# Kernel tuning notes

Measured on AMD Instinct MI355X. Metric: run time of the kernel, lower is better.

Reference implementation:

```python
import jax, jax.numpy as jnp
import numpy as np

# ---- static skeleton configuration ----
TOPOLOGY = [[0,1],[1,2],[2,3],[3,4],[0,5],[5,6],[6,7],[7,8],[0,9],[9,10],[10,11],[11,12],
            [12,13],[13,14],[12,15],[15,16],[16,17],[17,18],[18,19],[12,20],[20,21],[21,22],[22,23],[23,24]]
NEIGHBOUR_LIST = [[0,1,2,4,5,8,9,24],[0,1,2,3,4,8],[0,1,2,3],[1,2,3],[0,1,4,5,6,8,9,24],[0,4,5,6,7,8],
                  [4,5,6,7],[5,6,7],[0,1,4,5,8,9,10,24],[0,4,8,9,10,11],[8,9,10,11,12,14,19],
                  [9,10,11,12,13,14,15,19,20],[10,11,12,13,14,15,19,20],[11,12,13,14,19],
                  [10,11,12,13,14,15,16,19,20],[11,12,14,15,16,17,19],[14,15,16,17,18],[15,16,17,18],
                  [16,17,18],[10,11,12,13,14,15,19,20,21],[11,12,14,19,20,21,22],[19,20,21,22,23],
                  [20,21,22,23],[21,22,23],[0,4,8,24]]
JOINT_NUM, IN_C, OUT_C, K, STRIDE, PAD = 25, 200, 400, 3, 2, 1
GN_GROUPS, GN_EPS = 10, 1e-5

def build_mask(nbr_list, in_c, out_c, joint_num, k):
    cin, cout = in_c // joint_num, out_c // joint_num
    m = np.zeros((out_c, in_c, k), np.float32)
    for i, nbr in enumerate(nbr_list):
        cols = [j * cin + c for j in nbr for c in range(cin)]
        m[i * cout:(i + 1) * cout, cols, :] = 1.0
    return jnp.asarray(m)

def build_pool(edges, cpe):
    edge_num = len(edges) + 1
    deg = {}
    for a, b in edges:
        deg[a] = deg.get(a, 0) + 1; deg[b] = deg.get(b, 0) + 1
    seq_list = []
    def find_seq(j, seq):
        if deg[j] > 2 and j != 0:
            seq_list.append(seq); seq = []
        if deg[j] == 1:
            seq_list.append(seq); return
        for idx, (a, b) in enumerate(edges):
            if a == j:
                find_seq(b, seq + [idx])
    find_seq(0, [])
    pooling_list = []
    for seq in seq_list:
        if len(seq) % 2 == 1:
            pooling_list.append([seq[0]]); seq = seq[1:]
        for i in range(0, len(seq), 2):
            pooling_list.append([seq[i], seq[i + 1]])
    pooling_list.append([edge_num - 1])
    W = np.zeros((len(pooling_list) * cpe, edge_num * cpe), np.float32)
    for i, pair in enumerate(pooling_list):
        for j in pair:
            W[i * cpe:(i + 1) * cpe, j * cpe:(j + 1) * cpe] += np.eye(cpe, dtype=np.float32) / len(pair)
    return jnp.asarray(W)

MASK0 = build_mask(NEIGHBOUR_LIST, IN_C, IN_C, JOINT_NUM, K)    # extra conv in->in
MASK1 = build_mask(NEIGHBOUR_LIST, IN_C, OUT_C, JOINT_NUM, K)   # main conv in->out
MASK_SC = build_mask(NEIGHBOUR_LIST, IN_C, OUT_C, JOINT_NUM, 1) # shortcut k=1
POOL_W = build_pool(TOPOLOGY, OUT_C // JOINT_NUM)               # [224, 400]

def conv1d(x, w, b, stride, pad):
    if pad > 0:
        x = jnp.pad(x, ((0, 0), (0, 0), (pad, pad)), mode='reflect')
    y = jax.lax.conv_general_dilated(x, w, (stride,), 'VALID',
                                     dimension_numbers=('NCH', 'OIH', 'NCH'))
    return y + b[None, :, None]

def group_norm(x, gamma, beta):
    B, C, T = x.shape
    xg = x.reshape(B, GN_GROUPS, C // GN_GROUPS, T)
    mu = xg.mean((2, 3), keepdims=True)
    var = xg.var((2, 3), keepdims=True)
    xn = ((xg - mu) * jax.lax.rsqrt(var + GN_EPS)).reshape(B, C, T)
    return xn * gamma[None, :, None] + beta[None, :, None]

def prelu(x, a):
    return jnp.where(x >= 0, x, a[0] * x)

def setup_inputs() -> dict:
    key = jax.random.key(0)
    ks = jax.random.split(key, 8)
    return {
        'x': jax.random.normal(ks[0], (16, IN_C, 8192), jnp.float32),
        'w0': jax.random.normal(ks[1], (IN_C, IN_C, K), jnp.float32) * 0.05,
        'b0': jax.random.normal(ks[2], (IN_C,), jnp.float32) * 0.05,
        'a0': jnp.full((1,), 0.25, jnp.float32),
        'w1': jax.random.normal(ks[3], (OUT_C, IN_C, K), jnp.float32) * 0.05,
        'b1': jax.random.normal(ks[4], (OUT_C,), jnp.float32) * 0.05,
        'gn_gamma': jnp.ones((OUT_C,), jnp.float32),
        'gn_beta': jnp.zeros((OUT_C,), jnp.float32),
        'ws': jax.random.normal(ks[5], (OUT_C, IN_C, 1), jnp.float32) * 0.05,
        'bs': jax.random.normal(ks[6], (OUT_C,), jnp.float32) * 0.05,
        'a1': jnp.full((1,), 0.25, jnp.float32),
    }

def reference(x, w0, b0, a0, w1, b1, gn_gamma, gn_beta, ws, bs, a1):
    # residual branch: extra SkeletonConv + PReLU, SkeletonConv (stride 2), GroupNorm
    h = conv1d(x, w0 * MASK0, b0, 1, PAD)
    h = prelu(h, a0)
    h = conv1d(h, w1 * MASK1, b1, STRIDE, PAD)
    h = group_norm(h, gn_gamma, gn_beta)
    # shortcut: masked 1x1 conv, stride 2
    s = conv1d(x, ws * MASK_SC, bs, STRIDE, 0)
    out = h + s                                   # [B, 400, 4096]
    out = jnp.einsum('nc,bct->bnt', POOL_W, out)  # SkeletonPool mean -> [B, 224, 4096]
    return prelu(out, a1)
```

## Files before the change

### kernel.cpp

```cpp
#include <hip/hip_runtime.h>

#define BATCH 16
#define CIN   200
#define T1    8192
#define COUTC 400
#define TT2   4096
#define NJ    25
#define NGROUP 10
#define CPG   40
#define NPOOL 14
#define CROWB 528

typedef __attribute__((ext_vector_type(8))) short bf16x8;
typedef __attribute__((ext_vector_type(4))) float f32x4;

__constant__ int NBR_OFF[NJ + 1] = {0,8,14,18,21,29,35,39,42,50,56,63,72,80,85,94,101,106,110,113,122,129,134,138,141,145};
__constant__ int NBR[145] = {
 0,1,2,4,5,8,9,24,
 0,1,2,3,4,8,
 0,1,2,3,
 1,2,3,
 0,1,4,5,6,8,9,24,
 0,4,5,6,7,8,
 4,5,6,7,
 5,6,7,
 0,1,4,5,8,9,10,24,
 0,4,8,9,10,11,
 8,9,10,11,12,14,19,
 9,10,11,12,13,14,15,19,20,
 10,11,12,13,14,15,19,20,
 11,12,13,14,19,
 10,11,12,13,14,15,16,19,20,
 11,12,14,15,16,17,19,
 14,15,16,17,18,
 15,16,17,18,
 16,17,18,
 10,11,12,13,14,15,19,20,21,
 11,12,14,19,20,21,22,
 19,20,21,22,23,
 20,21,22,23,
 21,22,23,
 0,4,8,24};
__constant__ int PAIR_A[NPOOL] = {0,2,4,6,8,10,12,14,15,17,19,20,22,24};
__constant__ int PAIR_B[NPOOL] = {1,3,5,7,9,11,13,-1,16,18,-1,21,23,-1};
__constant__ int JSPLIT[5] = {0,6,12,18,25};
__constant__ int PUOFF[15] = {0,9,13,22,26,35,45,53,62,70,74,83,91,95,99};
__constant__ int PU[99] = {
 0,1,2,3,4,5,8,9,24,
 0,1,2,3,
 0,1,4,5,6,7,8,9,24,
 4,5,6,7,
 0,1,4,5,8,9,10,11,24,
 8,9,10,11,12,13,14,15,19,20,
 10,11,12,13,14,15,19,20,
 10,11,12,13,14,15,16,19,20,
 11,12,14,15,16,17,18,19,
 15,16,17,18,
 10,11,12,13,14,15,19,20,21,
 11,12,14,19,20,21,22,23,
 20,21,22,23,
 0,4,8,24};
__constant__ int PNMF[NPOOL] = {7,3,7,3,7,8,6,7,6,3,7,6,3,3};
__constant__ int FB0[NPOOL]  = {0,7,10,17,20,27,35,41,48,54,57,64,70,73};
__constant__ int FRAG_P[76] = {
 0,0,0,0,0,0,0, 1,1,1, 2,2,2,2,2,2,2, 3,3,3, 4,4,4,4,4,4,4, 5,5,5,5,5,5,5,5,
 6,6,6,6,6,6, 7,7,7,7,7,7,7, 8,8,8,8,8,8, 9,9,9, 10,10,10,10,10,10,10,
 11,11,11,11,11,11, 12,12,12, 13,13,13};
__constant__ int NSF[NJ] = {2,2,1,1,2,2,1,1,2,2,2,3,2,2,3,2,2,1,1,3,2,2,1,1,1};
__constant__ int FBS[NJ] = {0,2,4,5,6,8,10,11,12,14,16,18,21,23,25,28,30,32,33,34,37,39,41,42,43};
__constant__ int FRAG_SJ[44] = {
 0,0, 1,1, 2, 3, 4,4, 5,5, 6, 7, 8,8, 9,9, 10,10, 11,11,11, 12,12, 13,13,
 14,14,14, 15,15, 16,16, 17, 18, 19,19,19, 20,20, 21,21, 22, 23, 24};
#define NF1   (NJ * 7)
#define DSC_SC   304
#define DSC_C1   480
#define DSC_TOT  (DSC_C1 + NF1 * 4)

__device__ __forceinline__ unsigned bfround(float f) {
    unsigned u = __builtin_bit_cast(unsigned, f);
    return (u + 0x7FFFu + ((u >> 16) & 1u)) >> 16;
}
__device__ __forceinline__ unsigned packbf(float lo, float hi) {
    return bfround(lo) | (bfround(hi) << 16);
}
__device__ __forceinline__ float bflo(unsigned u) { return __builtin_bit_cast(float, u << 16); }
__device__ __forceinline__ float bfhi(unsigned u) { return __builtin_bit_cast(float, u & 0xFFFF0000u); }

__global__ void wprep1(const float* __restrict__ w1, unsigned short* __restrict__ wA)
{
    const int f  = blockIdx.x;
    const int jo = f / 7;
    const int mf = f - jo * 7;
    const int off = NBR_OFF[jo];
    const int deg = NBR_OFF[jo + 1] - off;
    for (int e = threadIdx.x; e < 512; e += 256) {
        int lane = e >> 3, j = e & 7;
        int m = lane & 15, kb = lane >> 4;
        int c8 = mf * 4 + kb;
        float v = 0.f;
        if (c8 < 3 * deg) {
            int tap = (c8 >= 2 * deg) ? 2 : ((c8 >= deg) ? 1 : 0);
            int nbr_i = c8 - tap * deg;
            int ci = NBR[off + nbr_i] * 8 + j;
            v = w1[(size_t)(jo * 16 + m) * 600 + ci * 3 + tap];
        }
        wA[(size_t)f * 512 + e] = (unsigned short)bfround(v);
    }
}

__global__ void wprep0(const float* __restrict__ w0, unsigned short* __restrict__ wA)
{
    const int f  = blockIdx.x;
    const int p  = FRAG_P[f];
    const int mf = f - FB0[p];
    const int puo = PUOFF[p];
    const int u   = PUOFF[p + 1] - puo;
    for (int e = threadIdx.x; e < 512; e += 256) {
        int lane = e >> 3, j = e & 7;
        int m = lane & 15, kb = lane >> 4;
        int c8 = mf * 4 + kb;
        int jm = (m < 8) ? PAIR_A[p] : PAIR_B[p];
        float v = 0.f;
        if (c8 < 3 * u && jm >= 0) {
            int tap = (c8 >= 2 * u) ? 2 : ((c8 >= u) ? 1 : 0);
            int ni  = c8 - tap * u;
            int nbr = PU[puo + ni];
            int offj = NBR_OFF[jm], degj = NBR_OFF[jm + 1] - offj;
            bool mem = false;
            for (int s = 0; s < degj; ++s) mem = mem || (NBR[offj + s] == nbr);
            if (mem) {
                int ci = nbr * 8 + j;
                v = w0[(size_t)(jm * 8 + (m & 7)) * 600 + ci * 3 + tap];
            }
        }
        wA[(size_t)f * 512 + e] = (unsigned short)bfround(v);
    }
}

__global__ void wprepS(const float* __restrict__ wsc, unsigned short* __restrict__ wA)
{
    const int f  = blockIdx.x;
    const int jo = FRAG_SJ[f];
    const int mf = f - FBS[jo];
    const int off = NBR_OFF[jo];
    const int deg = NBR_OFF[jo + 1] - off;
    for (int e = threadIdx.x; e < 512; e += 256) {
        int lane = e >> 3, j = e & 7;
        int m = lane & 15, kb = lane >> 4;
        int c8 = mf * 4 + kb;
        float v = 0.f;
        if (c8 < deg) {
            int ci = NBR[off + c8] * 8 + j;
            v = wsc[(size_t)(jo * 16 + m) * 200 + ci];
        }
        wA[(size_t)f * 512 + e] = (unsigned short)bfround(v);
    }
}

__global__ void dprep(int* __restrict__ dsc)
{
    for (int e = threadIdx.x; e < DSC_TOT; e += 256) {
        if (e < DSC_SC) {
            int f = e >> 2, q = e & 3;
            int p = FRAG_P[f], mf = f - FB0[p];
            int puo = PUOFF[p], u = PUOFF[p + 1] - puo;
            int c8 = mf * 4 + q;
            int tp = 0, ni = 0;
            if (c8 < 3 * u) {
                tp = (c8 >= 2 * u) ? 2 : ((c8 >= u) ? 1 : 0);
                ni = c8 - tp * u;
            }
            dsc[e] = (tp << 12) | (PU[puo + ni] * 16);
        } else if (e < DSC_C1) {
            int e2 = e - DSC_SC;
            int f = e2 >> 2, q = e2 & 3;
            int jo = FRAG_SJ[f], mf = f - FBS[jo];
            int off = NBR_OFF[jo], deg = NBR_OFF[jo + 1] - off;
            int c8 = mf * 4 + q;
            int ni = (c8 < deg) ? c8 : deg - 1;
            dsc[e] = NBR[off + ni] * 16;
        } else {
            int e2 = e - DSC_C1;
            int f = e2 >> 2, q = e2 & 3;
            int jo = f / 7, mf = f - jo * 7;
            int off = NBR_OFF[jo], deg = NBR_OFF[jo + 1] - off;
            int c8 = mf * 4 + q;
            int tp = 0, ni = 0;
            if (c8 < 3 * deg) {
                tp = (c8 >= 2 * deg) ? 2 : ((c8 >= deg) ? 1 : 0);
                ni = c8 - tp * deg;
            }
            int rowd = (tp == 1) ? 33 : (tp >> 1);
            dsc[e] = rowd * CROWB + NBR[off + ni] * 16;
        }
    }
}

__global__ __launch_bounds__(256) void conv0s_mfma(
    const float* __restrict__ x, const unsigned short* __restrict__ wA0,
    const unsigned short* __restrict__ wAs, const int* __restrict__ dsc,
    const float* __restrict__ b0, const float* __restrict__ a0,
    const float* __restrict__ bsc,
    unsigned short* __restrict__ h0T, unsigned short* __restrict__ sbu)
{
    __shared__ __align__(16) unsigned short xs[66 * 264];
    __shared__ int dl[DSC_C1];
    __shared__ float b0l[CIN], bscl[COUTC];
    const int b   = blockIdx.y;
    const int t0  = blockIdx.x * 64;
    const int tid = threadIdx.x;

    for (int i = tid; i < DSC_C1; i += 256) dl[i] = dsc[i];
    for (int i = tid; i < CIN; i += 256) b0l[i] = b0[i];
    for (int i = tid; i < COUTC; i += 256) bscl[i] = bsc[i];

    const float* xb = x + (size_t)b * CIN * T1;
    for (int e = tid; e < (CIN / 4) * 16; e += 256) {
        int c4 = e >> 4, k = e & 15;
        const float* xc = xb + (size_t)(4 * c4) * T1 + t0 + 4 * k;
        float4 v0 = *(const float4*)(xc);
        float4 v1 = *(const float4*)(xc + T1);
        float4 v2 = *(const float4*)(xc + 2 * T1);
        float4 v3 = *(const float4*)(xc + 3 * T1);
        char* base = (char*)xs + 8 * c4 + (4 * k + 1) * CROWB;
        *(uint2*)(base)             = make_uint2(packbf(v0.x, v1.x), packbf(v2.x, v3.x));
        *(uint2*)(base + CROWB)     = make_uint2(packbf(v0.y, v1.y), packbf(v2.y, v3.y));
        *(uint2*)(base + 2 * CROWB) = make_uint2(packbf(v0.z, v1.z), packbf(v2.z, v3.z));
        *(uint2*)(base + 3 * CROWB) = make_uint2(packbf(v0.w, v1.w), packbf(v2.w, v3.w));
    }
    for (int e = tid; e < 2 * CIN; e += 256) {
        int c = e >> 1, h = e & 1;
        int t = h ? (t0 + 64) : (t0 - 1);
        t = (t < 0) ? 1 : ((t >= T1) ? (2 * T1 - 2 - t) : t);
        float v = xb[(size_t)c * T1 + t];
        *(unsigned short*)((char*)xs + (h ? 65 : 0) * CROWB + 2 * c) = (unsigned short)bfround(v);
    }
    __syncthreads();

    const int w = tid >> 6, lane = tid & 63;
    const int q = lane >> 4, n = lane & 15;
    const float alpha = a0[0];
    const int ws2 = w & 1, wh = w >> 1;
    const int pbase = wh * 7;
    const int rA = ws2 * 32 + n;
    char* xsb = (char*)xs + rA * CROWB;

    unsigned h0k[7][2][2];
    for (int pi = 0; pi < 7; ++pi) {
        const int p = pbase + pi;
        const int fb = FB0[p], nmf = PNMF[p];
        const unsigned short* wAb = wA0 + (size_t)fb * 512;
        f32x4 acc0 = {0.f, 0.f, 0.f, 0.f};
        f32x4 acc1 = {0.f, 0.f, 0.f, 0.f};
        int i1 = (nmf > 1) ? 1 : 0;
        bf16x8 af0 = *(const bf16x8*)(wAb + (size_t)lane * 8);
        int d = dl[fb * 4 + q];
        bf16x8 b0v = *(const bf16x8*)(xsb + (d >> 12) * CROWB + (d & 0xFFF));
        bf16x8 b1v = *(const bf16x8*)(xsb + (d >> 12) * CROWB + (d & 0xFFF) + 16 * CROWB);
        bf16x8 af1 = *(const bf16x8*)(wAb + ((size_t)i1 * 64 + lane) * 8);
        d = dl[(fb + i1) * 4 + q];
        bf16x8 b0n = *(const bf16x8*)(xsb + (d >> 12) * CROWB + (d & 0xFFF));
        bf16x8 b1n = *(const bf16x8*)(xsb + (d >> 12) * CROWB + (d & 0xFFF) + 16 * CROWB);
        for (int mf = 0; mf < nmf; ++mf) {
            int m2 = (mf + 2 < nmf) ? mf + 2 : nmf - 1;
            bf16x8 a2 = *(const bf16x8*)(wAb + ((size_t)m2 * 64 + lane) * 8);
            d = dl[(fb + m2) * 4 + q];
            bf16x8 b02 = *(const bf16x8*)(xsb + (d >> 12) * CROWB + (d & 0xFFF));
            bf16x8 b12 = *(const bf16x8*)(xsb + (d >> 12) * CROWB + (d & 0xFFF) + 16 * CROWB);
            acc0 = __builtin_amdgcn_mfma_f32_16x16x32_bf16(af0, b0v, acc0, 0, 0, 0);
            acc1 = __builtin_amdgcn_mfma_f32_16x16x32_bf16(af0, b1v, acc1, 0, 0, 0);
            af0 = af1; af1 = a2;
            b0v = b0n; b0n = b02;
            b1v = b1n; b1n = b12;
        }
        int jm = (q < 2) ? PAIR_A[p] : PAIR_B[p];
        if (jm >= 0) {
            int ocb = (q & 1) * 4;
            float bb0 = b0l[jm * 8 + ocb + 0], bb1 = b0l[jm * 8 + ocb + 1];
            float bb2 = b0l[jm * 8 + ocb + 2], bb3 = b0l[jm * 8 + ocb + 3];
            float v0 = acc0[0] + bb0; v0 = (v0 >= 0.f) ? v0 : alpha * v0;
            float v1 = acc0[1] + bb1; v1 = (v1 >= 0.f) ? v1 : alpha * v1;
            float v2 = acc0[2] + bb2; v2 = (v2 >= 0.f) ? v2 : alpha * v2;
            float v3 = acc0[3] + bb3; v3 = (v3 >= 0.f) ? v3 : alpha * v3;
            h0k[pi][0][0] = packbf(v0, v1); h0k[pi][0][1] = packbf(v2, v3);
            v0 = acc1[0] + bb0; v0 = (v0 >= 0.f) ? v0 : alpha * v0;
            v1 = acc1[1] + bb1; v1 = (v1 >= 0.f) ? v1 : alpha * v1;
            v2 = acc1[2] + bb2; v2 = (v2 >= 0.f) ? v2 : alpha * v2;
            v3 = acc1[3] + bb3; v3 = (v3 >= 0.f) ? v3 : alpha * v3;
            h0k[pi][1][0] = packbf(v0, v1); h0k[pi][1][1] = packbf(v2, v3);
        }
    }

    for (int jo = w; jo < NJ; jo += 4) {
        const int fb = FBS[jo], nsf = NSF[jo];
        const unsigned short* wAb = wAs + (size_t)fb * 512;
        const int dbase = DSC_SC + fb * 4 + q;
        char* rb0 = (char*)xs + (2 * n + 1) * CROWB;
        f32x4 acc0 = {0.f, 0.f, 0.f, 0.f};
        f32x4 acc1 = {0.f, 0.f, 0.f, 0.f};
        int i1 = (nsf > 1) ? 1 : 0;
        bf16x8 af0 = *(const bf16x8*)(wAb + (size_t)lane * 8);
        int d = dl[dbase];
        bf16x8 b0v = *(const bf16x8*)(rb0 + d);
        bf16x8 b1v = *(const bf16x8*)(rb0 + d + 32 * CROWB);
        bf16x8 af1 = *(const bf16x8*)(wAb + ((size_t)i1 * 64 + lane) * 8);
        d = dl[dbase + i1 * 4];
        bf16x8 b0n = *(const bf16x8*)(rb0 + d);
        bf16x8 b1n = *(const bf16x8*)(rb0 + d + 32 * CROWB);
        for (int mf = 0; mf < nsf; ++mf) {
            int m2 = (mf + 2 < nsf) ? mf + 2 : nsf - 1;
            bf16x8 a2 = *(const bf16x8*)(wAb + ((size_t)m2 * 64 + lane) * 8);
            d = dl[dbase + m2 * 4];
            bf16x8 b02 = *(const bf16x8*)(rb0 + d);
            bf16x8 b12 = *(const bf16x8*)(rb0 + d + 32 * CROWB);
            acc0 = __builtin_amdgcn_mfma_f32_16x16x32_bf16(af0, b0v, acc0, 0, 0, 0);
            acc1 = __builtin_amdgcn_mfma_f32_16x16x32_bf16(af0, b1v, acc1, 0, 0, 0);
            af0 = af1; af1 = a2;
            b0v = b0n; b0n = b02;
            b1v = b1n; b1n = b12;
        }
        unsigned short* sp = sbu + ((size_t)b * COUTC + jo * 16 + q * 4) * TT2 + (t0 >> 1) + n;
#pragma unroll
        for (int r = 0; r < 4; ++r) {
            float bsv = bscl[jo * 16 + q * 4 + r];
            sp[(size_t)r * TT2]      = (unsigned short)bfround(acc0[r] + bsv);
            sp[(size_t)r * TT2 + 16] = (unsigned short)bfround(acc1[r] + bsv);
        }
    }

    __syncthreads();
    for (int pi = 0; pi < 7; ++pi) {
        int p = pbase + pi;
        int jm = (q < 2) ? PAIR_A[p] : PAIR_B[p];
        if (jm >= 0) {
            int cb = (jm * 8 + (q & 1) * 4) * 2;
            int rowb0 = rA * CROWB + cb;
            *(unsigned*)((char*)xs + rowb0)     = h0k[pi][0][0];
            *(unsigned*)((char*)xs + rowb0 + 4) = h0k[pi][0][1];
            int rowb1 = (rA + 16) * CROWB + cb;
            *(unsigned*)((char*)xs + rowb1)     = h0k[pi][1][0];
            *(unsigned*)((char*)xs + rowb1 + 4) = h0k[pi][1][1];
        }
    }
    __syncthreads();
    unsigned short* ho = h0T + ((size_t)b * T1 + t0 + w * 16) * CIN;
    for (int e = lane; e < 16 * 25; e += 64) {
        int row = e / 25, k = e - row * 25;
        uint4 u = *(const uint4*)((char*)xs + (w * 16 + row) * CROWB + 16 * k);
        *(uint4*)(ho + (size_t)row * CIN + 8 * k) = u;
    }
}

__global__ __launch_bounds__(256) void conv1_mfma(
    const unsigned short* __restrict__ h0T, const unsigned short* __restrict__ wA,
    const int* __restrict__ dsc, const float* __restrict__ b1,
    unsigned short* __restrict__ h1u, float* __restrict__ part)
{
    __shared__ __align__(16) unsigned short xs[65 * 264];
    __shared__ int dl1[NF1 * 4];
    __shared__ float biasl[COUTC];
    const int b   = blockIdx.y;
    const int t20 = blockIdx.x * 32;
    const int tid = threadIdx.x;

    for (int i = tid; i < NF1 * 4; i += 256) dl1[i] = dsc[DSC_C1 + i];
    for (int i = tid; i < COUTC; i += 256) biasl[i] = b1[i];

    const unsigned short* hTb = h0T + (size_t)b * T1 * CIN;
    for (int e = tid; e < 65 * 25; e += 256) {
        int row = e / 25, k = e - row * 25;
        int p = (row < 33) ? (2 * t20 - 1 + 2 * row) : (2 * t20 + 2 * (row - 33));
        if (p < 0) p = 1;
        uint4 u = *(const uint4*)(hTb + (size_t)p * CIN + 8 * k);
        *(uint4*)((char*)xs + row * CROWB + 16 * k) = u;
    }
    __syncthreads();

    const int w = tid >> 6, lane = tid & 63;
    const int q = lane >> 4, n = lane & 15;
    const int j0 = JSPLIT[w], j1 = JSPLIT[w + 1];
    const int t2gA = t20 + n, t2gB = t20 + 16 + n;
    char* xsb = (char*)xs + n * CROWB;

    for (int jo = j0; jo < j1; ++jo) {
        const unsigned short* wAb = wA + (size_t)(jo * 7) * 512;
        const int dbase = jo * 28 + q;
        f32x4 acc0 = {0.f, 0.f, 0.f, 0.f};
        f32x4 acc1 = {0.f, 0.f, 0.f, 0.f};
#pragma unroll
        for (int mf = 0; mf < 7; ++mf) {
            bf16x8 a = *(const bf16x8*)(wAb + ((size_t)mf * 64 + lane) * 8);
            int d = dl1[dbase + mf * 4];
            bf16x8 bb0 = *(const bf16x8*)(xsb + d);
            bf16x8 bb1 = *(const bf16x8*)(xsb + d + 16 * CROWB);
            acc0 = __builtin_amdgcn_mfma_f32_16x16x32_bf16(a, bb0, acc0, 0, 0, 0);
            acc1 = __builtin_amdgcn_mfma_f32_16x16x32_bf16(a, bb1, acc1, 0, 0, 0);
        }

        float s = 0.f, ss = 0.f;
        unsigned short* hout = h1u + ((size_t)b * COUTC + jo * 16) * TT2;
#pragma unroll
        for (int r = 0; r < 4; ++r) {
            int oc = q * 4 + r;
            float bv = biasl[jo * 16 + oc];
            float v0 = acc0[r] + bv;
            float v1 = acc1[r] + bv;
            s += v0 + v1; ss += v0 * v0 + v1 * v1;
            hout[(size_t)oc * TT2 + t2gA] = (unsigned short)bfround(v0);
            hout[(size_t)oc * TT2 + t2gB] = (unsigned short)bfround(v1);
        }
        for (int o2 = 1; o2 < 32; o2 <<= 1) {
            s  += __shfl_xor(s, o2, 64);
            ss += __shfl_xor(ss, o2, 64);
        }
        if ((lane & 31) == 0) {
            int half = lane >> 5;
            size_t o = (((size_t)b * 50 + jo * 2 + half) * 128 + blockIdx.x) * 2;
            part[o] = s; part[o + 1] = ss;
        }
    }
}

__global__ __launch_bounds__(256) void gn_final2(const float* __restrict__ part,
                                                 float* __restrict__ stats)
{
    const int bg = blockIdx.x;
    const int b = bg / NGROUP, g = bg % NGROUP;
    float s = 0.f, ss = 0.f;
    for (int k = threadIdx.x; k < 5 * 128; k += 256) {
        int sb = k >> 7, slot = k & 127;
        size_t o = (((size_t)b * 50 + g * 5 + sb) * 128 + slot) * 2;
        s += part[o]; ss += part[o + 1];
    }
    for (int o2 = 32; o2; o2 >>= 1) {
        s  += __shfl_down(s, o2, 64);
        ss += __shfl_down(ss, o2, 64);
    }
    __shared__ float rs[4], rss[4];
    const int lane = threadIdx.x & 63, wv = threadIdx.x >> 6;
    if (lane == 0) { rs[wv] = s; rss[wv] = ss; }
    __syncthreads();
    if (threadIdx.x == 0) {
        float S  = rs[0] + rs[1] + rs[2] + rs[3];
        float SS = rss[0] + rss[1] + rss[2] + rss[3];
        const float invN = 1.0f / (float)(CPG * TT2);
        float mean = S * invN;
        float var  = SS * invN - mean * mean;
        stats[bg * 2]     = mean;
        stats[bg * 2 + 1] = rsqrtf(var + 1e-5f);
    }
}

__global__ void gn_coef(const float* __restrict__ stats, const float* __restrict__ gamma,
                        const float* __restrict__ beta, float* __restrict__ AB)
{
    int idx = blockIdx.x * 256 + threadIdx.x;
    if (idx < BATCH * COUTC) {
        int b = idx / COUTC; int ch = idx - b * COUTC;
        int g = ch / CPG;
        float m = stats[(b * NGROUP + g) * 2];
        float r = stats[(b * NGROUP + g) * 2 + 1];
        float A = r * gamma[ch];
        AB[(size_t)idx * 2]     = A;
        AB[(size_t)idx * 2 + 1] = beta[ch] - m * A;
    }
}

__global__ __launch_bounds__(256) void final2pb(
    const unsigned* __restrict__ h1b, const unsigned* __restrict__ sb,
    const float* __restrict__ AB, const float* __restrict__ a1,
    float* __restrict__ outb)
{
    const int n     = blockIdx.y >> 1;
    const int chalf = blockIdx.y & 1;
    const int b     = blockIdx.z;
    const int tid   = threadIdx.x;
    const int t0    = (blockIdx.x * 256 + tid) * 4;

    int js[2];
    js[0] = PAIR_A[n];
    const int jb = PAIR_B[n];
    const int L = (jb >= 0) ? 2 : 1;
    js[1] = (jb >= 0) ? jb : js[0];

    __shared__ float Al[2][8], Bl[2][8];
    if (tid < 16) {
        int ji = tid >> 3, c8 = tid & 7;
        int ch = js[ji] * 16 + chalf * 8 + c8;
        Al[ji][c8] = AB[((size_t)b * COUTC + ch) * 2];
        Bl[ji][c8] = AB[((size_t)b * COUTC + ch) * 2 + 1];
    }
    __syncthreads();

    const float alpha = a1[0];
    const float invL  = (L == 2) ? 0.5f : 1.0f;

    float acc[8][4];
#pragma unroll
    for (int c = 0; c < 8; ++c)
#pragma unroll
        for (int i = 0; i < 4; ++i) acc[c][i] = 0.f;

    for (int ji = 0; ji < L; ++ji) {
        const int jc0 = js[ji] * 16 + chalf * 8;
#pragma unroll
        for (int c = 0; c < 8; ++c) {
            size_t rowoff = ((size_t)b * COUTC + jc0 + c) * (TT2 / 2) + t0 / 2;
            uint2 hv = *(const uint2*)(h1b + rowoff);
            uint2 sv = *(const uint2*)(sb + rowoff);
            float A = Al[ji][c], Bc = Bl[ji][c];
            acc[c][0] += bflo(hv.x) * A + Bc + bflo(sv.x);
            acc[c][1] += bfhi(hv.x) * A + Bc + bfhi(sv.x);
            acc[c][2] += bflo(hv.y) * A + Bc + bflo(sv.y);
            acc[c][3] += bfhi(hv.y) * A + Bc + bfhi(sv.y);
        }
    }

    float* ob = outb + ((size_t)b * 224 + n * 16 + chalf * 8) * TT2 + t0;
#pragma unroll
    for (int c = 0; c < 8; ++c) {
        float4 o;
#pragma unroll
        for (int i = 0; i < 4; ++i) {
            float v = acc[c][i] * invL;
            ((float*)&o)[i] = (v >= 0.f) ? v : alpha * v;
        }
        *(float4*)(ob + (size_t)c * TT2) = o;
    }
}

extern "C" void kernel_launch(void* const* d_in, const int* in_sizes, int n_in,
                              void* d_out, int out_size, void* d_ws, size_t ws_size,
                              hipStream_t stream) {
    const float* x     = (const float*)d_in[0];
    const float* w0    = (const float*)d_in[1];
    const float* b0    = (const float*)d_in[2];
    const float* a0    = (const float*)d_in[3];
    const float* w1    = (const float*)d_in[4];
    const float* b1    = (const float*)d_in[5];
    const float* gamma = (const float*)d_in[6];
    const float* beta  = (const float*)d_in[7];
    const float* wsc   = (const float*)d_in[8];
    const float* bsc   = (const float*)d_in[9];
    const float* a1    = (const float*)d_in[10];
    float* out = (float*)d_out;

    const size_t NB = (size_t)BATCH * CIN * T1;
    unsigned short* h0T  = (unsigned short*)d_ws;
    unsigned short* sbu  = h0T + NB;
    unsigned short* h1u  = sbu + NB;
    unsigned short* wA1  = h1u + NB;
    unsigned short* wA0p = wA1 + (size_t)NF1 * 512;
    unsigned short* wAsp = wA0p + (size_t)76 * 512;
    int* dsc     = (int*)(wAsp + (size_t)44 * 512);
    float* part  = (float*)(dsc + DSC_TOT);
    float* stats = part + (size_t)BATCH * 50 * 128 * 2;
    float* AB    = stats + BATCH * NGROUP * 2;

    wprep1<<<dim3(NF1), 256, 0, stream>>>(w1, wA1);
    wprep0<<<dim3(76), 256, 0, stream>>>(w0, wA0p);
    wprepS<<<dim3(44), 256, 0, stream>>>(wsc, wAsp);
    dprep<<<dim3(1), 256, 0, stream>>>(dsc);
    conv0s_mfma<<<dim3(T1 / 64, BATCH), 256, 0, stream>>>(x, wA0p, wAsp, dsc, b0, a0, bsc, h0T, sbu);
    conv1_mfma<<<dim3(TT2 / 32, BATCH), 256, 0, stream>>>(h0T, wA1, dsc, b1, h1u, part);
    gn_final2<<<dim3(BATCH * NGROUP), 256, 0, stream>>>(part, stats);
    gn_coef<<<dim3(25), 256, 0, stream>>>(stats, gamma, beta, AB);
    final2pb<<<dim3(TT2 / 1024, NPOOL * 2, BATCH), 256, 0, stream>>>((const unsigned*)h1u,
                                                                     (const unsigned*)sbu, AB, a1, out);
}
```

Measured before the change: 173.8 us.

## Fuse conv0 and strided conv1 into one kernel, recomputing halo row

Merges the first masked conv (plus shortcut) with the stride-2 conv1 so the PReLU'd h0 tile stays in shared memory instead of being written to and reread from a global h0T buffer. Each block now loads one extra left-halo input row and recomputes the one extra h0 time step (the halo) needed by the stride-2 conv, storing h0 rows in the even/odd-split layout conv1 expects. This removes a large intermediate round trip through global memory and one kernel launch. In exchange it adds redundant halo compute, more LDS use and more register pressure per block.

```diff
diff --git a/kernel.cpp b/kernel.cpp
--- a/kernel.cpp
+++ b/kernel.cpp
@@ -44,6 +44,8 @@
 __constant__ int PAIR_A[NPOOL] = {0,2,4,6,8,10,12,14,15,17,19,20,22,24};
 __constant__ int PAIR_B[NPOOL] = {1,3,5,7,9,11,13,-1,16,18,-1,21,23,-1};
 __constant__ int JSPLIT[5] = {0,6,12,18,25};
+__constant__ int EPB[4] = {0,4,7,11};
+__constant__ int EPE[4] = {4,7,11,14};
 __constant__ int PUOFF[15] = {0,9,13,22,26,35,45,53,62,70,74,83,91,95,99};
 __constant__ int PU[99] = {
  0,1,2,3,4,5,8,9,24,
@@ -196,23 +198,28 @@
     }
 }
 
-__global__ __launch_bounds__(256) void conv0s_mfma(
+__global__ __launch_bounds__(256) void conv01_mfma(
     const float* __restrict__ x, const unsigned short* __restrict__ wA0,
-    const unsigned short* __restrict__ wAs, const int* __restrict__ dsc,
+    const unsigned short* __restrict__ wAs, const unsigned short* __restrict__ wA1,
+    const int* __restrict__ dsc,
     const float* __restrict__ b0, const float* __restrict__ a0,
-    const float* __restrict__ bsc,
-    unsigned short* __restrict__ h0T, unsigned short* __restrict__ sbu)
-{
-    __shared__ __align__(16) unsigned short xs[66 * 264];
+    const float* __restrict__ bsc, const float* __restrict__ b1,
+    unsigned short* __restrict__ sbu, unsigned short* __restrict__ h1u,
+    float* __restrict__ part)
+{
+    __shared__ __align__(16) unsigned short xs[67 * 264];
     __shared__ int dl[DSC_C1];
-    __shared__ float b0l[CIN], bscl[COUTC];
+    __shared__ int dl1[NF1 * 4];
+    __shared__ float b0l[CIN], bscl[COUTC], b1l[COUTC];
     const int b   = blockIdx.y;
     const int t0  = blockIdx.x * 64;
     const int tid = threadIdx.x;
 
     for (int i = tid; i < DSC_C1; i += 256) dl[i] = dsc[i];
+    for (int i = tid; i < NF1 * 4; i += 256) dl1[i] = dsc[DSC_C1 + i];
     for (int i = tid; i < CIN; i += 256) b0l[i] = b0[i];
     for (int i = tid; i < COUTC; i += 256) bscl[i] = bsc[i];
+    for (int i = tid; i < COUTC; i += 256) b1l[i] = b1[i];
 
     const float* xb = x + (size_t)b * CIN * T1;
     for (int e = tid; e < (CIN / 4) * 16; e += 256) {
@@ -222,18 +229,19 @@
         float4 v1 = *(const float4*)(xc + T1);
         float4 v2 = *(const float4*)(xc + 2 * T1);
         float4 v3 = *(const float4*)(xc + 3 * T1);
-        char* base = (char*)xs + 8 * c4 + (4 * k + 1) * CROWB;
+        char* base = (char*)xs + 8 * c4 + (4 * k + 2) * CROWB;
         *(uint2*)(base)             = make_uint2(packbf(v0.x, v1.x), packbf(v2.x, v3.x));
         *(uint2*)(base + CROWB)     = make_uint2(packbf(v0.y, v1.y), packbf(v2.y, v3.y));
         *(uint2*)(base + 2 * CROWB) = make_uint2(packbf(v0.z, v1.z), packbf(v2.z, v3.z));
         *(uint2*)(base + 3 * CROWB) = make_uint2(packbf(v0.w, v1.w), packbf(v2.w, v3.w));
     }
-    for (int e = tid; e < 2 * CIN; e += 256) {
-        int c = e >> 1, h = e & 1;
-        int t = h ? (t0 + 64) : (t0 - 1);
-        t = (t < 0) ? 1 : ((t >= T1) ? (2 * T1 - 2 - t) : t);
+    for (int e = tid; e < 3 * CIN; e += 256) {
+        int c = e / 3, h = e - c * 3;
+        int t = (h == 2) ? (t0 + 64) : (t0 - 2 + h);
+        t = (t < 0) ? -t : ((t >= T1) ? (2 * T1 - 2 - t) : t);
         float v = xb[(size_t)c * T1 + t];
-        *(unsigned short*)((char*)xs + (h ? 65 : 0) * CROWB + 2 * c) = (unsigned short)bfround(v);
+        int row = (h == 2) ? 66 : h;
+        *(unsigned short*)((char*)xs + row * CROWB + 2 * c) = (unsigned short)bfround(v);
     }
     __syncthreads();
 
@@ -243,7 +251,7 @@
     const int ws2 = w & 1, wh = w >> 1;
     const int pbase = wh * 7;
     const int rA = ws2 * 32 + n;
-    char* xsb = (char*)xs + rA * CROWB;
+    char* xsb = (char*)xs + (rA + 1) * CROWB;
 
     unsigned h0k[7][2][2];
     for (int pi = 0; pi < 7; ++pi) {
@@ -291,11 +299,34 @@
         }
     }
 
+    unsigned h0e[4][2];
+    for (int pi = EPB[w]; pi < EPE[w]; ++pi) {
+        const int fb = FB0[pi], nmf = PNMF[pi];
+        const unsigned short* wAb = wA0 + (size_t)fb * 512;
+        f32x4 acc = {0.f, 0.f, 0.f, 0.f};
+        for (int mf = 0; mf < nmf; ++mf) {
+            bf16x8 a = *(const bf16x8*)(wAb + ((size_t)mf * 64 + lane) * 8);
+            int d = dl[(fb + mf) * 4 + q];
+            bf16x8 bv = *(const bf16x8*)((char*)xs + (n + (d >> 12)) * CROWB + (d & 0xFFF));
+            acc = __builtin_amdgcn_mfma_f32_16x16x32_bf16(a, bv, acc, 0, 0, 0);
+        }
+        int jm = (q < 2) ? PAIR_A[pi] : PAIR_B[pi];
+        int ei = pi - EPB[w];
+        if (jm >= 0) {
+            int ocb = (q & 1) * 4;
+            float v0 = acc[0] + b0l[jm * 8 + ocb + 0]; v0 = (v0 >= 0.f) ? v0 : alpha * v0;
+            float v1 = acc[1] + b0l[jm * 8 + ocb + 1]; v1 = (v1 >= 0.f) ? v1 : alpha * v1;
+            float v2 = acc[2] + b0l[jm * 8 + ocb + 2]; v2 = (v2 >= 0.f) ? v2 : alpha * v2;
+            float v3 = acc[3] + b0l[jm * 8 + ocb + 3]; v3 = (v3 >= 0.f) ? v3 : alpha * v3;
+            h0e[ei][0] = packbf(v0, v1); h0e[ei][1] = packbf(v2, v3);
+        }
+    }
+
     for (int jo = w; jo < NJ; jo += 4) {
         const int fb = FBS[jo], nsf = NSF[jo];
         const unsigned short* wAb = wAs + (size_t)fb * 512;
         const int dbase = DSC_SC + fb * 4 + q;
-        char* rb0 = (char*)xs + (2 * n + 1) * CROWB;
+        char* rb0 = (char*)xs + (2 * n + 2) * CROWB;
         f32x4 acc0 = {0.f, 0.f, 0.f, 0.f};
         f32x4 acc1 = {0.f, 0.f, 0.f, 0.f};
         int i1 = (nsf > 1) ? 1 : 0;
@@ -329,61 +360,48 @@
     }
 
     __syncthreads();
-    for (int pi = 0; pi < 7; ++pi) {
-        int p = pbase + pi;
-        int jm = (q < 2) ? PAIR_A[p] : PAIR_B[p];
-        if (jm >= 0) {
-            int cb = (jm * 8 + (q & 1) * 4) * 2;
-            int rowb0 = rA * CROWB + cb;
-            *(unsigned*)((char*)xs + rowb0)     = h0k[pi][0][0];
-            *(unsigned*)((char*)xs + rowb0 + 4) = h0k[pi][0][1];
-            int rowb1 = (rA + 16) * CROWB + cb;
-            *(unsigned*)((char*)xs + rowb1)     = h0k[pi][1][0];
-            *(unsigned*)((char*)xs + rowb1 + 4) = h0k[pi][1][1];
+    {
+        int h0r = rA + 1;
+        int rl0 = (h0r >> 1) + ((h0r & 1) ? 33 : 0);
+        int h1r = rA + 17;
+        int rl1 = (h1r >> 1) + ((h1r & 1) ? 33 : 0);
+        for (int pi = 0; pi < 7; ++pi) {
+            int p = pbase + pi;
+            int jm = (q < 2) ? PAIR_A[p] : PAIR_B[p];
+            if (jm >= 0) {
+                int cb = (jm * 8 + (q & 1) * 4) * 2;
+                char* d0 = (char*)xs + rl0 * CROWB + cb;
+                *(unsigned*)(d0)     = h0k[pi][0][0];
+                *(unsigned*)(d0 + 4) = h0k[pi][0][1];
+                char* d1 = (char*)xs + rl1 * CROWB + cb;
+                *(unsigned*)(d1)     = h0k[pi][1][0];
+                *(unsigned*)(d1 + 4) = h0k[pi][1][1];
+            }
+        }
+        int rle = (n >> 1) + ((n & 1) ? 33 : 0);
+        for (int pi = EPB[w]; pi < EPE[w]; ++pi) {
+            int jm = (q < 2) ? PAIR_A[pi] : PAIR_B[pi];
+            if (jm >= 0) {
+                int cb = (jm * 8 + (q & 1) * 4) * 2;
+                char* de = (char*)xs + rle * CROWB + cb;
+                *(unsigned*)(de)     = h0e[pi - EPB[w]][0];
+                *(unsigned*)(de + 4) = h0e[pi - EPB[w]][1];
+            }
         }
     }
     __syncthreads();
-    unsigned short* ho = h0T + ((size_t)b * T1 + t0 + w * 16) * CIN;
-    for (int e = lane; e < 16 * 25; e += 64) {
-        int row = e / 25, k = e - row * 25;
-        uint4 u = *(const uint4*)((char*)xs + (w * 16 + row) * CROWB + 16 * k);
-        *(uint4*)(ho + (size_t)row * CIN + 8 * k) = u;
-    }
-}
-
-__global__ __launch_bounds__(256) void conv1_mfma(
-    const unsigned short* __restrict__ h0T, const unsigned short* __restrict__ wA,
-    const int* __restrict__ dsc, const float* __restrict__ b1,
-    unsigned short* __restrict__ h1u, float* __restrict__ part)
-{
-    __shared__ __align__(16) unsigned short xs[65 * 264];
-    __shared__ int dl1[NF1 * 4];
-    __shared__ float biasl[COUTC];
-    const int b   = blockIdx.y;
+    if (blockIdx.x == 0) {
+        for (int i = tid; i < CIN; i += 256) xs[i] = xs[264 + i];
+    }
+    __syncthreads();
+
     const int t20 = blockIdx.x * 32;
-    const int tid = threadIdx.x;
-
-    for (int i = tid; i < NF1 * 4; i += 256) dl1[i] = dsc[DSC_C1 + i];
-    for (int i = tid; i < COUTC; i += 256) biasl[i] = b1[i];
-
-    const unsigned short* hTb = h0T + (size_t)b * T1 * CIN;
-    for (int e = tid; e < 65 * 25; e += 256) {
-        int row = e / 25, k = e - row * 25;
-        int p = (row < 33) ? (2 * t20 - 1 + 2 * row) : (2 * t20 + 2 * (row - 33));
-        if (p < 0) p = 1;
-        uint4 u = *(const uint4*)(hTb + (size_t)p * CIN + 8 * k);
-        *(uint4*)((char*)xs + row * CROWB + 16 * k) = u;
-    }
-    __syncthreads();
-
-    const int w = tid >> 6, lane = tid & 63;
-    const int q = lane >> 4, n = lane & 15;
     const int j0 = JSPLIT[w], j1 = JSPLIT[w + 1];
     const int t2gA = t20 + n, t2gB = t20 + 16 + n;
-    char* xsb = (char*)xs + n * CROWB;
+    char* xsb1 = (char*)xs + n * CROWB;
 
     for (int jo = j0; jo < j1; ++jo) {
-        const unsigned short* wAb = wA + (size_t)(jo * 7) * 512;
+        const unsigned short* wAb = wA1 + (size_t)(jo * 7) * 512;
         const int dbase = jo * 28 + q;
         f32x4 acc0 = {0.f, 0.f, 0.f, 0.f};
         f32x4 acc1 = {0.f, 0.f, 0.f, 0.f};
@@ -391,8 +409,8 @@
         for (int mf = 0; mf < 7; ++mf) {
             bf16x8 a = *(const bf16x8*)(wAb + ((size_t)mf * 64 + lane) * 8);
             int d = dl1[dbase + mf * 4];
-            bf16x8 bb0 = *(const bf16x8*)(xsb + d);
-            bf16x8 bb1 = *(const bf16x8*)(xsb + d + 16 * CROWB);
+            bf16x8 bb0 = *(const bf16x8*)(xsb1 + d);
+            bf16x8 bb1 = *(const bf16x8*)(xsb1 + d + 16 * CROWB);
             acc0 = __builtin_amdgcn_mfma_f32_16x16x32_bf16(a, bb0, acc0, 0, 0, 0);
             acc1 = __builtin_amdgcn_mfma_f32_16x16x32_bf16(a, bb1, acc1, 0, 0, 0);
         }
@@ -402,7 +420,7 @@
 #pragma unroll
         for (int r = 0; r < 4; ++r) {
             int oc = q * 4 + r;
-            float bv = biasl[jo * 16 + oc];
+            float bv = b1l[jo * 16 + oc];
             float v0 = acc0[r] + bv;
             float v1 = acc1[r] + bv;
             s += v0 + v1; ss += v0 * v0 + v1 * v1;
@@ -546,8 +564,7 @@
     float* out = (float*)d_out;
 
     const size_t NB = (size_t)BATCH * CIN * T1;
-    unsigned short* h0T  = (unsigned short*)d_ws;
-    unsigned short* sbu  = h0T + NB;
+    unsigned short* sbu  = (unsigned short*)d_ws;
     unsigned short* h1u  = sbu + NB;
     unsigned short* wA1  = h1u + NB;
     unsigned short* wA0p = wA1 + (size_t)NF1 * 512;
@@ -561,8 +578,8 @@
     wprep0<<<dim3(76), 256, 0, stream>>>(w0, wA0p);
     wprepS<<<dim3(44), 256, 0, stream>>>(wsc, wAsp);
     dprep<<<dim3(1), 256, 0, stream>>>(dsc);
-    conv0s_mfma<<<dim3(T1 / 64, BATCH), 256, 0, stream>>>(x, wA0p, wAsp, dsc, b0, a0, bsc, h0T, sbu);
-    conv1_mfma<<<dim3(TT2 / 32, BATCH), 256, 0, stream>>>(h0T, wA1, dsc, b1, h1u, part);
+    conv01_mfma<<<dim3(T1 / 64, BATCH), 256, 0, stream>>>(x, wA0p, wAsp, wA1, dsc,
+                                                          b0, a0, bsc, b1, sbu, h1u, part);
     gn_final2<<<dim3(BATCH * NGROUP), 256, 0, stream>>>(part, stats);
     gn_coef<<<dim3(25), 256, 0, stream>>>(stats, gamma, beta, AB);
     final2pb<<<dim3(TT2 / 1024, NPOOL * 2, BATCH), 256, 0, stream>>>((const unsigned*)h1u,
```

Measured after the change: 192.4 us. +10.7%, slower.
